# Optimization experiments

Measured on AMD Instinct MI355X. Metric: run time of the kernel, lower is better.

The kernel has to match this reference:

```python
import jax, jax.numpy as jnp
import numpy as np

B, T, H, W, D, NH = 8, 16, 14, 14, 768, 12
HID = int(D * 4.0)
HEAD_DIM = D // NH
EPS = 1e-5


def _ln(x, w, b):
    m = x.mean(-1, keepdims=True)
    v = ((x - m) ** 2).mean(-1, keepdims=True)
    return (x - m) * jax.lax.rsqrt(v + EPS) * w + b


def _attn(x, qkv_w, proj_w, proj_b):
    # x: [Bn, S, D]; qkv_w: [D, 3D] (no bias); proj: [D, D] + bias
    Bn, S, _ = x.shape
    qkv = (x @ qkv_w).reshape(Bn, S, 3, NH, HEAD_DIM).transpose(2, 0, 3, 1, 4)
    q, k, v = qkv[0], qkv[1], qkv[2]
    a = jnp.einsum('bhqd,bhkd->bhqk', q, k) * (HEAD_DIM ** -0.5)
    a = jax.nn.softmax(a, axis=-1)
    o = jnp.einsum('bhqk,bhkd->bhqd', a, v).transpose(0, 2, 1, 3).reshape(Bn, S, D)
    return o @ proj_w + proj_b


def setup_inputs() -> dict:
    key = jax.random.key(0)
    ks = jax.random.split(key, 20)
    N = H * W * T
    s = 0.02
    f32 = jnp.float32
    return {
        'x': jax.random.normal(ks[0], (B, 1 + N, D), f32),
        'tn1_w': jnp.ones((D,), f32), 'tn1_b': jnp.zeros((D,), f32),
        't_qkv_w': jax.random.normal(ks[1], (D, 3 * D), f32) * s,
        't_proj_w': jax.random.normal(ks[2], (D, D), f32) * s,
        't_proj_b': jnp.zeros((D,), f32),
        'tfc_w': jax.random.normal(ks[3], (D, D), f32) * s,
        'tfc_b': jnp.zeros((D,), f32),
        'n1_w': jnp.ones((D,), f32), 'n1_b': jnp.zeros((D,), f32),
        's_qkv_w': jax.random.normal(ks[4], (D, 3 * D), f32) * s,
        's_proj_w': jax.random.normal(ks[5], (D, D), f32) * s,
        's_proj_b': jnp.zeros((D,), f32),
        'n2_w': jnp.ones((D,), f32), 'n2_b': jnp.zeros((D,), f32),
        'fc1_w': jax.random.normal(ks[6], (D, HID), f32) * s,
        'fc1_b': jnp.zeros((HID,), f32),
        'fc2_w': jax.random.normal(ks[7], (HID, D), f32) * s,
        'fc2_b': jnp.zeros((D,), f32),
        'pt_mask': jnp.ones((B, 1 + N), dtype=bool),
        't_frames': T, 'height': H, 'width': W,
    }


def reference(x, tn1_w, tn1_b, t_qkv_w, t_proj_w, t_proj_b, tfc_w, tfc_b,
              n1_w, n1_b, s_qkv_w, s_proj_w, s_proj_b, n2_w, n2_b,
              fc1_w, fc1_b, fc2_w, fc2_b, pt_mask, t_frames, height, width):
    # divided space-time attention; USE_CLS_TOKEN=True, use_pt_visibility=False
    b = x.shape[0]
    t, h, w = t_frames, height, width
    n = h * w * t
    # --- temporal attention over t per (b, h, w) ---
    xt = x[:, 1:, :].reshape(b * h * w, t, D)  # 'b (h w t) m -> (b h w) t m'
    rt = _attn(_ln(xt, tn1_w, tn1_b), t_qkv_w, t_proj_w, t_proj_b)
    rt = rt.reshape(b, n, D) @ tfc_w + tfc_b  # temporal_fc
    xt2 = x[:, 1:, :] + rt
    init_cls = x[:, 0:1, :]  # [b, 1, D]
    # --- spatial attention over (1 + h*w) per (b, t) ---
    cls_tok = jnp.broadcast_to(init_cls, (b, t, D)).reshape(b * t, 1, D)
    xs = xt2.reshape(b, h * w, t, D).transpose(0, 2, 1, 3).reshape(b * t, h * w, D)
    xs = jnp.concatenate([cls_tok, xs], axis=1)  # [(b t), 1+hw, D]
    rs = _attn(_ln(xs, n1_w, n1_b), s_qkv_w, s_proj_w, s_proj_b)
    cls_out = rs[:, 0, :].reshape(b, t, D).mean(axis=1, keepdims=True)
    rs = rs[:, 1:, :].reshape(b, t, h * w, D).transpose(0, 2, 1, 3).reshape(b, n, D)
    x_new = jnp.concatenate([init_cls, xt2], axis=1) + jnp.concatenate([cls_out, rs], axis=1)
    # --- MLP block ---
    y = _ln(x_new, n2_w, n2_b)
    y = jax.nn.gelu(y @ fc1_w + fc1_b, approximate=False) @ fc2_w + fc2_b
    return x_new + y
```

## Files before the change

### kernel.cpp

```cpp
#include <hip/hip_runtime.h>
#include <cstdint>

using u16 = unsigned short;
using u32 = unsigned int;

typedef __bf16 bf16x8 __attribute__((ext_vector_type(8)));
typedef float  floatx4 __attribute__((ext_vector_type(4)));

#define DEV static __device__ __forceinline__

DEV u16 f2bf(float f) {
    u32 u = __float_as_uint(f);
    u += 0x7FFFu + ((u >> 16) & 1u);
    return (u16)(u >> 16);
}
DEV float bf2f(u16 v) { return __uint_as_float(((u32)v) << 16); }

DEV floatx4 mfma32(bf16x8 a, bf16x8 b, floatx4 c) {
    return __builtin_amdgcn_mfma_f32_16x16x32_bf16(a, b, c, 0, 0, 0);
}

DEV floatx4 fzero() { floatx4 z; z[0]=0.f; z[1]=0.f; z[2]=0.f; z[3]=0.f; return z; }

typedef __attribute__((address_space(3))) u32 as3_u32;
typedef __attribute__((address_space(1))) u32 as1_u32;

DEV void async_ld16(const u16* g, u16* l) {
    __builtin_amdgcn_global_load_lds(
        (const as1_u32*)g, (as3_u32*)l, 16, 0, 0);
}

__global__ __launch_bounds__(256) void transpose_w(
    const float* __restrict__ W, u16* __restrict__ Wt, int K, int N)
{
    __shared__ float t[32][33];
    const int tx = threadIdx.x, ty = threadIdx.y;
    const int gx = blockIdx.x * 32;
    const int gy = blockIdx.y * 32;
    #pragma unroll
    for (int i = 0; i < 4; ++i)
        t[ty + i*8][tx] = W[(size_t)(gy + ty + i*8) * N + gx + tx];
    __syncthreads();
    #pragma unroll
    for (int i = 0; i < 4; ++i)
        Wt[(size_t)(gx + ty + i*8) * K + gy + tx] = f2bf(t[tx][ty + i*8]);
}

__global__ __launch_bounds__(256) void cast_bf16(
    const float* __restrict__ W, u16* __restrict__ o, int n4)
{
    const int i = blockIdx.x * 256 + threadIdx.x;
    if (i < n4) {
        float4 v = reinterpret_cast<const float4*>(W)[i];
        union { u16 u[4]; uint2 q; } r;
        r.u[0]=f2bf(v.x); r.u[1]=f2bf(v.y); r.u[2]=f2bf(v.z); r.u[3]=f2bf(v.w);
        reinterpret_cast<uint2*>(o)[i] = r.q;
    }
}

__global__ __launch_bounds__(256) void fuse_bias(
    const float* __restrict__ pb, const float* __restrict__ Wf,
    const float* __restrict__ bf, float* __restrict__ bc)
{
    const int n = blockIdx.x * 4 + (threadIdx.x >> 6);
    const int lane = threadIdx.x & 63;
    float s = 0.f;
    #pragma unroll
    for (int it = 0; it < 12; ++it) {
        const int j = it*64 + lane;
        s += pb[j] * Wf[(size_t)j * 768 + n];
    }
    #pragma unroll
    for (int o = 32; o > 0; o >>= 1) s += __shfl_xor(s, o);
    if (lane == 0) bc[n] = s + bf[n];
}

template<int MODE>
__global__ __launch_bounds__(256) void ln_kernel(
    const float* __restrict__ xp, const u16* __restrict__ xt2,
    const float* __restrict__ w, const float* __restrict__ b,
    u16* __restrict__ out, int nrows)
{
    const int row = blockIdx.x * 4 + (threadIdx.x >> 6);
    if (row >= nrows) return;
    const int lane = threadIdx.x & 63;
    float vals[12];
    if constexpr (MODE == 0) {
        const float* src = xp + (size_t)(row + row/3136 + 1) * 768;
        #pragma unroll
        for (int j = 0; j < 3; ++j) {
            float4 v = reinterpret_cast<const float4*>(src)[j*64 + lane];
            vals[j*4+0]=v.x; vals[j*4+1]=v.y; vals[j*4+2]=v.z; vals[j*4+3]=v.w;
        }
    } else {
        const int bt = row / 197;
        const int p  = row - bt * 197;
        const int b0 = bt >> 4, tt = bt & 15;
        if (p == 0) {
            const float* src = xp + (size_t)b0 * 3137 * 768;
            #pragma unroll
            for (int j = 0; j < 3; ++j) {
                float4 v = reinterpret_cast<const float4*>(src)[j*64 + lane];
                vals[j*4+0]=v.x; vals[j*4+1]=v.y; vals[j*4+2]=v.z; vals[j*4+3]=v.w;
            }
        } else {
            const u16* src = xt2 + (size_t)(b0*3136 + (p-1)*16 + tt) * 768;
            #pragma unroll
            for (int j = 0; j < 3; ++j) {
                uint2 q = reinterpret_cast<const uint2*>(src)[j*64 + lane];
                vals[j*4+0] = bf2f((u16)(q.x & 0xFFFF));
                vals[j*4+1] = bf2f((u16)(q.x >> 16));
                vals[j*4+2] = bf2f((u16)(q.y & 0xFFFF));
                vals[j*4+3] = bf2f((u16)(q.y >> 16));
            }
        }
    }
    float s = 0.f, ss = 0.f;
    #pragma unroll
    for (int e = 0; e < 12; ++e) { s += vals[e]; ss += vals[e]*vals[e]; }
    #pragma unroll
    for (int o = 32; o > 0; o >>= 1) { s += __shfl_xor(s, o); ss += __shfl_xor(ss, o); }
    const float mean = s * (1.f/768.f);
    const float var  = ss * (1.f/768.f) - mean*mean;
    const float rstd = rsqrtf(var + 1e-5f);
    #pragma unroll
    for (int j = 0; j < 3; ++j) {
        const int c4 = (j*64 + lane) * 4;
        union { u16 u[4]; uint2 q; } o;
        #pragma unroll
        for (int e = 0; e < 4; ++e)
            o.u[e] = f2bf((vals[j*4+e] - mean)*rstd*w[c4+e] + b[c4+e]);
        *reinterpret_cast<uint2*>(&out[(size_t)row*768 + c4]) = o.q;
    }
}

__global__ __launch_bounds__(256) void combine_ln2(
    const float* __restrict__ xp, const u16* __restrict__ xt2,
    const u16* __restrict__ rsb, const float* __restrict__ w, const float* __restrict__ b,
    float* __restrict__ xnew, u16* __restrict__ ln2, int nrows)
{
    const int row = blockIdx.x * 4 + (threadIdx.x >> 6);
    if (row >= nrows) return;
    const int lane = threadIdx.x & 63;
    const int b0 = row / 3137;
    const int j  = row - b0 * 3137;
    float vals[12];
    if (j == 0) {
        #pragma unroll
        for (int e = 0; e < 12; ++e) {
            const int c = e*64 + lane;
            float acc = 0.f;
            for (int t = 0; t < 16; ++t)
                acc += bf2f(rsb[(size_t)(b0*16 + t) * 197 * 768 + c]);
            vals[e] = xp[(size_t)row*768 + c] + acc * (1.f/16.f);
        }
    } else {
        const int n_idx = j - 1;
        const int hw = n_idx >> 4, tt = n_idx & 15;
        const u16* a  = xt2 + (size_t)(b0*3136 + n_idx) * 768;
        const u16* r2 = rsb + (size_t)((b0*16 + tt)*197 + 1 + hw) * 768;
        #pragma unroll
        for (int e = 0; e < 12; ++e) {
            const int c = e*64 + lane;
            vals[e] = bf2f(a[c]) + bf2f(r2[c]);
        }
    }
    float s = 0.f, ss = 0.f;
    #pragma unroll
    for (int e = 0; e < 12; ++e) { s += vals[e]; ss += vals[e]*vals[e]; }
    #pragma unroll
    for (int o = 32; o > 0; o >>= 1) { s += __shfl_xor(s, o); ss += __shfl_xor(ss, o); }
    const float mean = s * (1.f/768.f);
    const float var  = ss * (1.f/768.f) - mean*mean;
    const float rstd = rsqrtf(var + 1e-5f);
    #pragma unroll
    for (int e = 0; e < 12; ++e) {
        const int c = e*64 + lane;
        xnew[(size_t)row*768 + c] = vals[e];
        ln2[(size_t)row*768 + c]  = f2bf((vals[e] - mean)*rstd*w[c] + b[c]);
    }
}

template<int RESID, bool BIAS, bool GELU_ACT, bool OUTF, bool OUTB, bool MASKM>
__global__ __launch_bounds__(256) void gemm_bt(
    const u16* __restrict__ A, const u16* __restrict__ Bt,
    const float* __restrict__ bias, const float* __restrict__ resid,
    float* __restrict__ Cf, u16* __restrict__ Cb,
    int N, int K, int lda, int ldb, int Mvalid)
{
    __shared__ __attribute__((aligned(16))) u16 smem[4*128*32];
    const int tid  = threadIdx.x;
    const int wave = tid >> 6;
    const int lane = tid & 63;
    const int m15  = lane & 15;
    const int quad = lane >> 4;
    const int wm = wave >> 1, wn = wave & 1;

    const int gx = (int)gridDim.x;
    const int nwg = gx * (int)gridDim.y;
    int lid = (int)blockIdx.y * gx + (int)blockIdx.x;
    {
        const int q = nwg >> 3, r = nwg & 7;
        const int c = lid & 7, idx = lid >> 3;
        lid = (c < r ? c*(q+1) : r*(q+1) + (c-r)*q) + idx;
    }
    const int bx = lid % gx;
    const int by = lid / gx;
    const long m0 = (long)by * 128;
    const long n0 = (long)bx * 128;

    const int s0 = wave*128 + lane;
    const int s1 = s0 + 64;
    const int kc0 = (s0 & 3) ^ ((s0 >> 3) & 3);
    const int kc1 = (s1 & 3) ^ ((s1 >> 3) & 3);
    const u16* Ag0 = A  + (size_t)(m0 + (s0 >> 2)) * lda + kc0 * 8;
    const u16* Ag1 = A  + (size_t)(m0 + (s1 >> 2)) * lda + kc1 * 8;
    const u16* Bg0 = Bt + (size_t)(n0 + (s0 >> 2)) * ldb + kc0 * 8;
    const u16* Bg1 = Bt + (size_t)(n0 + (s1 >> 2)) * ldb + kc1 * 8;

    const int swz = (quad ^ ((m15 >> 1) & 3)) * 8;

    floatx4 acc[4][4];
    #pragma unroll
    for (int i = 0; i < 4; ++i)
        #pragma unroll
        for (int j = 0; j < 4; ++j) acc[i][j] = fzero();

    auto stg = [&](int k0, int dn) {
        u16* base = smem + dn*8192;
        async_ld16(Ag0 + k0, base + (wave*2+0)*512);
        async_ld16(Ag1 + k0, base + (wave*2+1)*512);
        async_ld16(Bg0 + k0, base + 4096 + (wave*2+0)*512);
        async_ld16(Bg1 + k0, base + 4096 + (wave*2+1)*512);
    };
    auto comp = [&](int dn) {
        const u16* base = smem + dn*8192;
        bf16x8 af[4], bfr[4];
        #pragma unroll
        for (int i = 0; i < 4; ++i)
            af[i] = *reinterpret_cast<const bf16x8*>(&base[(wm*64 + i*16 + m15)*32 + swz]);
        #pragma unroll
        for (int j = 0; j < 4; ++j)
            bfr[j] = *reinterpret_cast<const bf16x8*>(&base[4096 + (wn*64 + j*16 + m15)*32 + swz]);
        #pragma unroll
        for (int i = 0; i < 4; ++i)
            #pragma unroll
            for (int j = 0; j < 4; ++j)
                acc[i][j] = mfma32(af[i], bfr[j], acc[i][j]);
    };

    const int NK = K >> 5;
    stg(0, 0);
    __syncthreads();
    for (int k = 0; k < NK; k += 2) {
        stg((k+1) << 5, 1);
        comp(0);
        __syncthreads();
        if (k + 2 < NK) stg((k+2) << 5, 0);
        comp(1);
        __syncthreads();
    }

    float bv[4];
    #pragma unroll
    for (int j = 0; j < 4; ++j)
        bv[j] = BIAS ? bias[n0 + wn*64 + j*16 + m15] : 0.f;

    if constexpr (OUTB) {
        u16* cbuf = smem + wave * 2048;
        #pragma unroll
        for (int p = 0; p < 2; ++p) {
            __syncthreads();
            #pragma unroll
            for (int ii = 0; ii < 2; ++ii) {
                const int i = p*2 + ii;
                #pragma unroll
                for (int j = 0; j < 4; ++j) {
                    #pragma unroll
                    for (int r = 0; r < 4; ++r) {
                        const long row = m0 + wm*64 + i*16 + quad*4 + r;
                        float v = acc[i][j][r] + bv[j];
                        if constexpr (RESID == 1)
                            v += resid[(size_t)row * N + (n0 + wn*64 + j*16 + m15)];
                        if constexpr (RESID == 2)
                            v += resid[(size_t)(row + row/3136 + 1) * 768 + (n0 + wn*64 + j*16 + m15)];
                        if constexpr (GELU_ACT)
                            v = 0.5f * v * (1.f + erff(v * 0.70710678118f));
                        cbuf[(ii*16 + quad*4 + r)*64 + j*16 + m15] = f2bf(v);
                    }
                }
            }
            __syncthreads();
            #pragma unroll
            for (int it = 0; it < 4; ++it) {
                const int lr = (lane >> 3) + it*8;
                const int cc = lane & 7;
                const uint4 val = *reinterpret_cast<const uint4*>(&cbuf[lr*64 + cc*8]);
                const long grow = m0 + wm*64 + p*32 + lr;
                *reinterpret_cast<uint4*>(&Cb[(size_t)grow * N + n0 + wn*64 + cc*8]) = val;
            }
        }
    } else {
        #pragma unroll
        for (int j = 0; j < 4; ++j) {
            const long col = n0 + wn*64 + j*16 + m15;
            #pragma unroll
            for (int i = 0; i < 4; ++i) {
                const long rowb = m0 + wm*64 + i*16 + quad*4;
                #pragma unroll
                for (int r = 0; r < 4; ++r) {
                    const long row = rowb + r;
                    if constexpr (MASKM) { if (row >= Mvalid) continue; }
                    float v = acc[i][j][r] + bv[j];
                    if constexpr (RESID == 1) v += resid[(size_t)row * N + col];
                    if constexpr (RESID == 2) v += resid[(size_t)(row + row/3136 + 1) * 768 + col];
                    if constexpr (GELU_ACT)   v = 0.5f * v * (1.f + erff(v * 0.70710678118f));
                    if constexpr (OUTF) Cf[(size_t)row * N + col] = v;
                }
            }
        }
    }
}

template<int S, int NQ, int NIT>
__global__ __launch_bounds__(256) void attn_kernel(
    const u16* __restrict__ qkv, u16* __restrict__ out, int ntask)
{
    __shared__ __attribute__((aligned(16))) u16 P_lds[4][16*32];
    const int wave = threadIdx.x >> 6;
    const int lane = threadIdx.x & 63;
    const int task = blockIdx.x * 4 + wave;
    if (task >= ntask) return;
    const int seq  = task / (12 * NQ);
    const int rem  = task - seq * (12 * NQ);
    const int head = rem / NQ;
    const int qt   = rem - head * NQ;
    const int m15  = lane & 15;
    const int quad = lane >> 4;
    const size_t base = (size_t)seq * S;

    const u16* qp = qkv + (base + qt*16 + m15) * 2304 + head*64 + quad*8;
    const bf16x8 Qf0 = *reinterpret_cast<const bf16x8*>(qp);
    const bf16x8 Qf1 = *reinterpret_cast<const bf16x8*>(qp + 32);

    floatx4 Oacc[4];
    #pragma unroll
    for (int c = 0; c < 4; ++c) Oacc[c] = fzero();
    float mrun = -__builtin_inff();
    float lrun = 0.f;
    u16* P = &P_lds[wave][0];

    for (int it = 0; it < NIT; ++it) {
        const int j0 = it * 32;
        floatx4 st[2];
        #pragma unroll
        for (int h2 = 0; h2 < 2; ++h2) {
            const u16* kp = qkv + (base + j0 + h2*16 + m15) * 2304 + 768 + head*64 + quad*8;
            const bf16x8 K0 = *reinterpret_cast<const bf16x8*>(kp);
            const bf16x8 K1 = *reinterpret_cast<const bf16x8*>(kp + 32);
            floatx4 z = fzero();
            z = mfma32(K0, Qf0, z);
            st[h2] = mfma32(K1, Qf1, z);
        }
        float sc[8];
        #pragma unroll
        for (int h2 = 0; h2 < 2; ++h2)
            #pragma unroll
            for (int r = 0; r < 4; ++r) {
                const int jj = j0 + h2*16 + quad*4 + r;
                sc[h2*4+r] = (jj < S) ? st[h2][r] * 0.125f : -__builtin_inff();
            }
        float tmax = sc[0];
        #pragma unroll
        for (int k = 1; k < 8; ++k) tmax = fmaxf(tmax, sc[k]);
        tmax = fmaxf(tmax, __shfl_xor(tmax, 16));
        tmax = fmaxf(tmax, __shfl_xor(tmax, 32));
        const float mnew = fmaxf(mrun, tmax);
        float p[8], tsum = 0.f;
        #pragma unroll
        for (int k = 0; k < 8; ++k) { p[k] = __expf(sc[k] - mnew); tsum += p[k]; }
        tsum += __shfl_xor(tsum, 16);
        tsum += __shfl_xor(tsum, 32);
        const float alpha = __expf(mrun - mnew);
        lrun = lrun * alpha + tsum;
        mrun = mnew;
        #pragma unroll
        for (int r = 0; r < 4; ++r) {
            const float ar = __shfl(alpha, quad*4 + r);
            #pragma unroll
            for (int c = 0; c < 4; ++c) Oacc[c][r] *= ar;
        }
        #pragma unroll
        for (int h2 = 0; h2 < 2; ++h2)
            #pragma unroll
            for (int r = 0; r < 4; ++r)
                P[m15*32 + h2*16 + quad*4 + r] = f2bf(p[h2*4+r]);
        const bf16x8 Pf = *reinterpret_cast<const bf16x8*>(&P[m15*32 + quad*8]);
        #pragma unroll
        for (int c = 0; c < 4; ++c) {
            union { u16 u[8]; bf16x8 v; } vf;
            #pragma unroll
            for (int jj2 = 0; jj2 < 8; ++jj2)
                vf.u[jj2] = qkv[(base + j0 + quad*8 + jj2) * 2304 + 1536 + head*64 + c*16 + m15];
            Oacc[c] = mfma32(Pf, vf.v, Oacc[c]);
        }
    }
    const float linv_self = 1.f / lrun;
    #pragma unroll
    for (int r = 0; r < 4; ++r) {
        const int prow = qt*16 + quad*4 + r;
        const float linv = __shfl(linv_self, quad*4 + r);
        if (prow < S) {
            u16* op = out + (base + prow) * 768 + head*64 + m15;
            #pragma unroll
            for (int c = 0; c < 4; ++c) op[c*16] = f2bf(Oacc[c][r] * linv);
        }
    }
}

extern "C" void kernel_launch(void* const* d_in, const int* in_sizes, int n_in,
                              void* d_out, int out_size, void* d_ws, size_t ws_size,
                              hipStream_t stream)
{
    (void)in_sizes; (void)n_in; (void)out_size; (void)ws_size;
    const float* x        = (const float*)d_in[0];
    const float* tn1_w    = (const float*)d_in[1];
    const float* tn1_b    = (const float*)d_in[2];
    const float* t_qkv_w  = (const float*)d_in[3];
    const float* t_proj_w = (const float*)d_in[4];
    const float* t_proj_b = (const float*)d_in[5];
    const float* tfc_w    = (const float*)d_in[6];
    const float* tfc_b    = (const float*)d_in[7];
    const float* n1_w     = (const float*)d_in[8];
    const float* n1_b     = (const float*)d_in[9];
    const float* s_qkv_w  = (const float*)d_in[10];
    const float* s_proj_w = (const float*)d_in[11];
    const float* s_proj_b = (const float*)d_in[12];
    const float* n2_w     = (const float*)d_in[13];
    const float* n2_b     = (const float*)d_in[14];
    const float* fc1_w    = (const float*)d_in[15];
    const float* fc1_b    = (const float*)d_in[16];
    const float* fc2_w    = (const float*)d_in[17];
    const float* fc2_b    = (const float*)d_in[18];
    float* out = (float*)d_out;

    char* ws = (char*)d_ws;
    size_t off = 0;
    auto alloc = [&](size_t bytes) -> void* {
        void* p = ws + off;
        off += (bytes + 255) & ~(size_t)255;
        return p;
    };
    u16* wt_tqkv  = (u16*)alloc((size_t)768*2304*2);
    u16* tproj_rm = (u16*)alloc((size_t)768*768*2);
    u16* wt_tfc   = (u16*)alloc((size_t)768*768*2);
    u16* wt_comb  = (u16*)alloc((size_t)768*768*2);
    float* bcomb  = (float*)alloc((size_t)768*4);
    u16* wt_sqkv  = (u16*)alloc((size_t)768*2304*2);
    u16* wt_sproj = (u16*)alloc((size_t)768*768*2);
    u16* wt_fc1   = (u16*)alloc((size_t)768*3072*2);
    u16* wt_fc2   = (u16*)alloc((size_t)3072*768*2);
    u16* slotA = (u16*)alloc((size_t)25280*2304*2);
    u16* slotB = (u16*)alloc((size_t)25216*768*2);
    u16* slotD = (u16*)alloc((size_t)25216*768*2);
    u16* slotE = (u16*)alloc((size_t)25216*768*2);

    dim3 tb(32, 8);
    transpose_w<<<dim3(72, 24), tb, 0, stream>>>(t_qkv_w,  wt_tqkv,  768, 2304);
    transpose_w<<<dim3(24, 24), tb, 0, stream>>>(tfc_w,    wt_tfc,   768, 768);
    transpose_w<<<dim3(72, 24), tb, 0, stream>>>(s_qkv_w,  wt_sqkv,  768, 2304);
    transpose_w<<<dim3(24, 24), tb, 0, stream>>>(s_proj_w, wt_sproj, 768, 768);
    transpose_w<<<dim3(96, 24), tb, 0, stream>>>(fc1_w,    wt_fc1,   768, 3072);
    transpose_w<<<dim3(24, 96), tb, 0, stream>>>(fc2_w,    wt_fc2,   3072, 768);
    cast_bf16<<<576, 256, 0, stream>>>(t_proj_w, tproj_rm, 768*768/4);

    gemm_bt<0,false,false,false,true,false><<<dim3(6,6), 256, 0, stream>>>(
        wt_tfc, tproj_rm, nullptr, nullptr, nullptr, wt_comb, 768, 768, 768, 768, 0);
    fuse_bias<<<192, 256, 0, stream>>>(t_proj_b, tfc_w, tfc_b, bcomb);

    u16* lnT  = slotD;
    u16* qkvT = slotA;
    ln_kernel<0><<<25088/4, 256, 0, stream>>>(x, nullptr, tn1_w, tn1_b, lnT, 25088);
    gemm_bt<0,false,false,false,true,false><<<dim3(18,196), 256, 0, stream>>>(
        lnT, wt_tqkv, nullptr, nullptr, nullptr, qkvT, 2304, 768, 768, 768, 0);

    u16* attnT = slotD;
    attn_kernel<16,1,1><<<18816/4, 256, 0, stream>>>(qkvT, attnT, 18816);

    u16* xt2 = slotB;
    gemm_bt<2,true,false,false,true,false><<<dim3(6,196), 256, 0, stream>>>(
        attnT, wt_comb, bcomb, x, nullptr, xt2, 768, 768, 768, 768, 0);

    u16* lnS = slotD;
    ln_kernel<1><<<25216/4, 256, 0, stream>>>(x, xt2, n1_w, n1_b, lnS, 25216);

    u16* qkvS = slotA;
    gemm_bt<0,false,false,false,true,false><<<dim3(18,197), 256, 0, stream>>>(
        lnS, wt_sqkv, nullptr, nullptr, nullptr, qkvS, 2304, 768, 768, 768, 0);

    u16* attnS = slotD;
    attn_kernel<197,13,7><<<19968/4, 256, 0, stream>>>(qkvS, attnS, 19968);

    u16* rsb = slotE;
    gemm_bt<0,true,false,false,true,false><<<dim3(6,197), 256, 0, stream>>>(
        attnS, wt_sproj, s_proj_b, nullptr, nullptr, rsb, 768, 768, 768, 768, 0);

    float* xnew = out;
    u16* ln2 = slotD;
    combine_ln2<<<25096/4, 256, 0, stream>>>(x, xt2, rsb, n2_w, n2_b, xnew, ln2, 25096);

    u16* h1 = slotA;
    for (int half = 0; half < 2; ++half) {
        const u16* w1h = wt_fc1 + (size_t)half * 1536 * 768;
        const float* b1h = fc1_b + half * 1536;
        gemm_bt<0,true,true,false,true,false><<<dim3(12,197), 256, 0, stream>>>(
            ln2, w1h, b1h, nullptr, nullptr, h1, 1536, 768, 768, 768, 0);
        const u16* w2h = wt_fc2 + (size_t)half * 1536;
        if (half == 0)
            gemm_bt<1,true,false,true,false,true><<<dim3(6,197), 256, 0, stream>>>(
                h1, w2h, fc2_b, out, out, nullptr, 768, 1536, 1536, 3072, 25096);
        else
            gemm_bt<1,false,false,true,false,true><<<dim3(6,197), 256, 0, stream>>>(
                h1, w2h, nullptr, out, out, nullptr, 768, 1536, 1536, 3072, 25096);
    }
}
```

Before: 1.302 ms.

## Load GEMM fragments directly from global memory into registers, bypassing LDS

The GEMM kernel drops the async global-to-LDS staging and the shared-memory double buffer. Each wave now loads its MFMA operand fragments straight from global memory into registers, with a two-stage register prefetch. This removes the block-wide barriers and LDS reads in the main loop, and the epilogue barriers. In exchange, each operand row is fetched by multiple waves, raising L1/L2 traffic, and the loads are narrow strided row accesses.

```diff
diff --git a/kernel.cpp b/kernel.cpp
--- a/kernel.cpp
+++ b/kernel.cpp
@@ -21,14 +21,6 @@
 }
 
 DEV floatx4 fzero() { floatx4 z; z[0]=0.f; z[1]=0.f; z[2]=0.f; z[3]=0.f; return z; }
-
-typedef __attribute__((address_space(3))) u32 as3_u32;
-typedef __attribute__((address_space(1))) u32 as1_u32;
-
-DEV void async_ld16(const u16* g, u16* l) {
-    __builtin_amdgcn_global_load_lds(
-        (const as1_u32*)g, (as3_u32*)l, 16, 0, 0);
-}
 
 __global__ __launch_bounds__(256) void transpose_w(
     const float* __restrict__ W, u16* __restrict__ Wt, int K, int N)
@@ -182,13 +174,13 @@
 }
 
 template<int RESID, bool BIAS, bool GELU_ACT, bool OUTF, bool OUTB, bool MASKM>
-__global__ __launch_bounds__(256) void gemm_bt(
+__global__ __launch_bounds__(256) void gemm_l2(
     const u16* __restrict__ A, const u16* __restrict__ Bt,
     const float* __restrict__ bias, const float* __restrict__ resid,
     float* __restrict__ Cf, u16* __restrict__ Cb,
     int N, int K, int lda, int ldb, int Mvalid)
 {
-    __shared__ __attribute__((aligned(16))) u16 smem[4*128*32];
+    __shared__ __attribute__((aligned(16))) u16 cbuf_all[4*2048];
     const int tid  = threadIdx.x;
     const int wave = tid >> 6;
     const int lane = tid & 63;
@@ -209,16 +201,12 @@
     const long m0 = (long)by * 128;
     const long n0 = (long)bx * 128;
 
-    const int s0 = wave*128 + lane;
-    const int s1 = s0 + 64;
-    const int kc0 = (s0 & 3) ^ ((s0 >> 3) & 3);
-    const int kc1 = (s1 & 3) ^ ((s1 >> 3) & 3);
-    const u16* Ag0 = A  + (size_t)(m0 + (s0 >> 2)) * lda + kc0 * 8;
-    const u16* Ag1 = A  + (size_t)(m0 + (s1 >> 2)) * lda + kc1 * 8;
-    const u16* Bg0 = Bt + (size_t)(n0 + (s0 >> 2)) * ldb + kc0 * 8;
-    const u16* Bg1 = Bt + (size_t)(n0 + (s1 >> 2)) * ldb + kc1 * 8;
-
-    const int swz = (quad ^ ((m15 >> 1) & 3)) * 8;
+    const u16* pAf[4]; const u16* pBf[4];
+    #pragma unroll
+    for (int f = 0; f < 4; ++f) {
+        pAf[f] = A  + (size_t)(m0 + wm*64 + f*16 + m15) * lda + quad*8;
+        pBf[f] = Bt + (size_t)(n0 + wn*64 + f*16 + m15) * ldb + quad*8;
+    }
 
     floatx4 acc[4][4];
     #pragma unroll
@@ -226,51 +214,45 @@
         #pragma unroll
         for (int j = 0; j < 4; ++j) acc[i][j] = fzero();
 
-    auto stg = [&](int k0, int dn) {
-        u16* base = smem + dn*8192;
-        async_ld16(Ag0 + k0, base + (wave*2+0)*512);
-        async_ld16(Ag1 + k0, base + (wave*2+1)*512);
-        async_ld16(Bg0 + k0, base + 4096 + (wave*2+0)*512);
-        async_ld16(Bg1 + k0, base + 4096 + (wave*2+1)*512);
+    bf16x8 a0[4], b0[4], a1[4], b1[4];
+    auto LD = [&](bf16x8* av, bf16x8* bv, int k0) {
+        #pragma unroll
+        for (int f = 0; f < 4; ++f)
+            av[f] = *reinterpret_cast<const bf16x8*>(pAf[f] + k0);
+        #pragma unroll
+        for (int f = 0; f < 4; ++f)
+            bv[f] = *reinterpret_cast<const bf16x8*>(pBf[f] + k0);
     };
-    auto comp = [&](int dn) {
-        const u16* base = smem + dn*8192;
-        bf16x8 af[4], bfr[4];
+    auto MM = [&](bf16x8* av, bf16x8* bv) {
         #pragma unroll
         for (int i = 0; i < 4; ++i)
-            af[i] = *reinterpret_cast<const bf16x8*>(&base[(wm*64 + i*16 + m15)*32 + swz]);
-        #pragma unroll
-        for (int j = 0; j < 4; ++j)
-            bfr[j] = *reinterpret_cast<const bf16x8*>(&base[4096 + (wn*64 + j*16 + m15)*32 + swz]);
-        #pragma unroll
-        for (int i = 0; i < 4; ++i)
             #pragma unroll
             for (int j = 0; j < 4; ++j)
-                acc[i][j] = mfma32(af[i], bfr[j], acc[i][j]);
+                acc[i][j] = mfma32(av[i], bv[j], acc[i][j]);
     };
 
-    const int NK = K >> 5;
-    stg(0, 0);
-    __syncthreads();
-    for (int k = 0; k < NK; k += 2) {
-        stg((k+1) << 5, 1);
-        comp(0);
-        __syncthreads();
-        if (k + 2 < NK) stg((k+2) << 5, 0);
-        comp(1);
-        __syncthreads();
-    }
-
-    float bv[4];
+    const int NK2 = K >> 6;
+    LD(a0, b0, 0);
+    int k0 = 0;
+    for (int it = 0; it < NK2 - 1; ++it, k0 += 64) {
+        LD(a1, b1, k0 + 32);
+        MM(a0, b0);
+        LD(a0, b0, k0 + 64);
+        MM(a1, b1);
+    }
+    LD(a1, b1, k0 + 32);
+    MM(a0, b0);
+    MM(a1, b1);
+
+    float bv4[4];
     #pragma unroll
     for (int j = 0; j < 4; ++j)
-        bv[j] = BIAS ? bias[n0 + wn*64 + j*16 + m15] : 0.f;
+        bv4[j] = BIAS ? bias[n0 + wn*64 + j*16 + m15] : 0.f;
 
     if constexpr (OUTB) {
-        u16* cbuf = smem + wave * 2048;
+        u16* cbuf = cbuf_all + wave * 2048;
         #pragma unroll
         for (int p = 0; p < 2; ++p) {
-            __syncthreads();
             #pragma unroll
             for (int ii = 0; ii < 2; ++ii) {
                 const int i = p*2 + ii;
@@ -279,7 +261,7 @@
                     #pragma unroll
                     for (int r = 0; r < 4; ++r) {
                         const long row = m0 + wm*64 + i*16 + quad*4 + r;
-                        float v = acc[i][j][r] + bv[j];
+                        float v = acc[i][j][r] + bv4[j];
                         if constexpr (RESID == 1)
                             v += resid[(size_t)row * N + (n0 + wn*64 + j*16 + m15)];
                         if constexpr (RESID == 2)
@@ -290,7 +272,6 @@
                     }
                 }
             }
-            __syncthreads();
             #pragma unroll
             for (int it = 0; it < 4; ++it) {
                 const int lr = (lane >> 3) + it*8;
@@ -311,7 +292,7 @@
                 for (int r = 0; r < 4; ++r) {
                     const long row = rowb + r;
                     if constexpr (MASKM) { if (row >= Mvalid) continue; }
-                    float v = acc[i][j][r] + bv[j];
+                    float v = acc[i][j][r] + bv4[j];
                     if constexpr (RESID == 1) v += resid[(size_t)row * N + col];
                     if constexpr (RESID == 2) v += resid[(size_t)(row + row/3136 + 1) * 768 + col];
                     if constexpr (GELU_ACT)   v = 0.5f * v * (1.f + erff(v * 0.70710678118f));
@@ -474,35 +455,35 @@
     transpose_w<<<dim3(24, 96), tb, 0, stream>>>(fc2_w,    wt_fc2,   3072, 768);
     cast_bf16<<<576, 256, 0, stream>>>(t_proj_w, tproj_rm, 768*768/4);
 
-    gemm_bt<0,false,false,false,true,false><<<dim3(6,6), 256, 0, stream>>>(
+    gemm_l2<0,false,false,false,true,false><<<dim3(6,6), 256, 0, stream>>>(
         wt_tfc, tproj_rm, nullptr, nullptr, nullptr, wt_comb, 768, 768, 768, 768, 0);
     fuse_bias<<<192, 256, 0, stream>>>(t_proj_b, tfc_w, tfc_b, bcomb);
 
     u16* lnT  = slotD;
     u16* qkvT = slotA;
     ln_kernel<0><<<25088/4, 256, 0, stream>>>(x, nullptr, tn1_w, tn1_b, lnT, 25088);
-    gemm_bt<0,false,false,false,true,false><<<dim3(18,196), 256, 0, stream>>>(
+    gemm_l2<0,false,false,false,true,false><<<dim3(18,196), 256, 0, stream>>>(
         lnT, wt_tqkv, nullptr, nullptr, nullptr, qkvT, 2304, 768, 768, 768, 0);
 
     u16* attnT = slotD;
     attn_kernel<16,1,1><<<18816/4, 256, 0, stream>>>(qkvT, attnT, 18816);
 
     u16* xt2 = slotB;
-    gemm_bt<2,true,false,false,true,false><<<dim3(6,196), 256, 0, stream>>>(
+    gemm_l2<2,true,false,false,true,false><<<dim3(6,196), 256, 0, stream>>>(
         attnT, wt_comb, bcomb, x, nullptr, xt2, 768, 768, 768, 768, 0);
 
     u16* lnS = slotD;
     ln_kernel<1><<<25216/4, 256, 0, stream>>>(x, xt2, n1_w, n1_b, lnS, 25216);
 
     u16* qkvS = slotA;
-    gemm_bt<0,false,false,false,true,false><<<dim3(18,197), 256, 0, stream>>>(
+    gemm_l2<0,false,false,false,true,false><<<dim3(18,197), 256, 0, stream>>>(
         lnS, wt_sqkv, nullptr, nullptr, nullptr, qkvS, 2304, 768, 768, 768, 0);
 
     u16* attnS = slotD;
     attn_kernel<197,13,7><<<19968/4, 256, 0, stream>>>(qkvS, attnS, 19968);
 
     u16* rsb = slotE;
-    gemm_bt<0,true,false,false,true,false><<<dim3(6,197), 256, 0, stream>>>(
+    gemm_l2<0,true,false,false,true,false><<<dim3(6,197), 256, 0, stream>>>(
         attnS, wt_sproj, s_proj_b, nullptr, nullptr, rsb, 768, 768, 768, 768, 0);
 
     float* xnew = out;
@@ -513,14 +494,14 @@
     for (int half = 0; half < 2; ++half) {
         const u16* w1h = wt_fc1 + (size_t)half * 1536 * 768;
         const float* b1h = fc1_b + half * 1536;
-        gemm_bt<0,true,true,false,true,false><<<dim3(12,197), 256, 0, stream>>>(
+        gemm_l2<0,true,true,false,true,false><<<dim3(12,197), 256, 0, stream>>>(
             ln2, w1h, b1h, nullptr, nullptr, h1, 1536, 768, 768, 768, 0);
         const u16* w2h = wt_fc2 + (size_t)half * 1536;
         if (half == 0)
-            gemm_bt<1,true,false,true,false,true><<<dim3(6,197), 256, 0, stream>>>(
+            gemm_l2<1,true,false,true,false,true><<<dim3(6,197), 256, 0, stream>>>(
                 h1, w2h, fc2_b, out, out, nullptr, 768, 1536, 1536, 3072, 25096);
         else
-            gemm_bt<1,false,false,true,false,true><<<dim3(6,197), 256, 0, stream>>>(
+            gemm_l2<1,false,false,true,false,true><<<dim3(6,197), 256, 0, stream>>>(
                 h1, w2h, nullptr, out, out, nullptr, 768, 1536, 1536, 3072, 25096);
     }
 }
```

Result: slower. 2.379 ms (+82.8%).

## Replace 4-wave 128x128 GEMM with single-wave 64x64 barrier-free GEMM

Applied to the files above, without the earlier changes.

Each GEMM workgroup becomes one 64-thread wave computing a 64x64 tile. Double-buffered LDS staging is synchronised with explicit vmcnt waits instead of __syncthreads, with a two-stage prefetch, and grids are resized to match. This removes workgroup barriers and shrinks LDS per block so more blocks fit per CU. In exchange, each block reuses less data per load, which raises global/L2 traffic, and the vmcnt-only waits rely on each lane reading only LDS it staged itself.

```diff
diff --git a/kernel.cpp b/kernel.cpp
--- a/kernel.cpp
+++ b/kernel.cpp
@@ -181,22 +181,24 @@
     }
 }
 
+#define WAITV8() do { asm volatile("s_waitcnt vmcnt(8)" ::: "memory"); \
+    __builtin_amdgcn_sched_barrier(0); } while(0)
+#define WAITVZ() do { asm volatile("s_waitcnt vmcnt(0)" ::: "memory"); \
+    __builtin_amdgcn_sched_barrier(0); } while(0)
+
 template<int RESID, bool BIAS, bool GELU_ACT, bool OUTF, bool OUTB, bool MASKM>
-__global__ __launch_bounds__(256) void gemm_bt(
+__global__ __launch_bounds__(64) void gemm_w(
     const u16* __restrict__ A, const u16* __restrict__ Bt,
     const float* __restrict__ bias, const float* __restrict__ resid,
     float* __restrict__ Cf, u16* __restrict__ Cb,
     int N, int K, int lda, int ldb, int Mvalid)
 {
-    __shared__ __attribute__((aligned(16))) u16 smem[4*128*32];
-    const int tid  = threadIdx.x;
-    const int wave = tid >> 6;
-    const int lane = tid & 63;
+    __shared__ __attribute__((aligned(16))) u16 smem[8192];
+    const int lane = threadIdx.x;
     const int m15  = lane & 15;
     const int quad = lane >> 4;
-    const int wm = wave >> 1, wn = wave & 1;
-
-    const int gx = (int)gridDim.x;
+
+    const int gx  = (int)gridDim.x;
     const int nwg = gx * (int)gridDim.y;
     int lid = (int)blockIdx.y * gx + (int)blockIdx.x;
     {
@@ -206,17 +208,24 @@
     }
     const int bx = lid % gx;
     const int by = lid / gx;
-    const long m0 = (long)by * 128;
-    const long n0 = (long)bx * 128;
-
-    const int s0 = wave*128 + lane;
-    const int s1 = s0 + 64;
-    const int kc0 = (s0 & 3) ^ ((s0 >> 3) & 3);
-    const int kc1 = (s1 & 3) ^ ((s1 >> 3) & 3);
-    const u16* Ag0 = A  + (size_t)(m0 + (s0 >> 2)) * lda + kc0 * 8;
-    const u16* Ag1 = A  + (size_t)(m0 + (s1 >> 2)) * lda + kc1 * 8;
-    const u16* Bg0 = Bt + (size_t)(n0 + (s0 >> 2)) * ldb + kc0 * 8;
-    const u16* Bg1 = Bt + (size_t)(n0 + (s1 >> 2)) * ldb + kc1 * 8;
+    const long m0 = (long)by * 64;
+    const long n0 = (long)bx * 64;
+
+    const u16* gA[4]; const u16* gB[4];
+    #pragma unroll
+    for (int i = 0; i < 4; ++i) {
+        const int s  = i*64 + lane;
+        const int kc = (s & 3) ^ ((s >> 3) & 3);
+        gA[i] = A  + (size_t)(m0 + (s >> 2)) * lda + kc*8;
+        gB[i] = Bt + (size_t)(n0 + (s >> 2)) * ldb + kc*8;
+    }
+    auto stg = [&](int k0, int d) {
+        u16* base = smem + d*4096;
+        #pragma unroll
+        for (int i = 0; i < 4; ++i) async_ld16(gA[i] + k0, base + i*512);
+        #pragma unroll
+        for (int i = 0; i < 4; ++i) async_ld16(gB[i] + k0, base + 2048 + i*512);
+    };
 
     const int swz = (quad ^ ((m15 >> 1) & 3)) * 8;
 
@@ -226,22 +235,15 @@
         #pragma unroll
         for (int j = 0; j < 4; ++j) acc[i][j] = fzero();
 
-    auto stg = [&](int k0, int dn) {
-        u16* base = smem + dn*8192;
-        async_ld16(Ag0 + k0, base + (wave*2+0)*512);
-        async_ld16(Ag1 + k0, base + (wave*2+1)*512);
-        async_ld16(Bg0 + k0, base + 4096 + (wave*2+0)*512);
-        async_ld16(Bg1 + k0, base + 4096 + (wave*2+1)*512);
-    };
-    auto comp = [&](int dn) {
-        const u16* base = smem + dn*8192;
+    auto comp = [&](int d) {
+        const u16* base = smem + d*4096;
         bf16x8 af[4], bfr[4];
         #pragma unroll
-        for (int i = 0; i < 4; ++i)
-            af[i] = *reinterpret_cast<const bf16x8*>(&base[(wm*64 + i*16 + m15)*32 + swz]);
+        for (int f = 0; f < 4; ++f)
+            af[f] = *reinterpret_cast<const bf16x8*>(&base[(f*16 + m15)*32 + swz]);
         #pragma unroll
         for (int j = 0; j < 4; ++j)
-            bfr[j] = *reinterpret_cast<const bf16x8*>(&base[4096 + (wn*64 + j*16 + m15)*32 + swz]);
+            bfr[j] = *reinterpret_cast<const bf16x8*>(&base[2048 + (j*16 + m15)*32 + swz]);
         #pragma unroll
         for (int i = 0; i < 4; ++i)
             #pragma unroll
@@ -251,26 +253,30 @@
 
     const int NK = K >> 5;
     stg(0, 0);
-    __syncthreads();
-    for (int k = 0; k < NK; k += 2) {
-        stg((k+1) << 5, 1);
+    stg(32, 1);
+    #pragma unroll 1
+    for (int t = 0; t + 4 <= NK; t += 2) {
+        WAITV8();
         comp(0);
-        __syncthreads();
-        if (k + 2 < NK) stg((k+2) << 5, 0);
+        __builtin_amdgcn_sched_barrier(0);
+        stg((t + 2) << 5, 0);
+        WAITV8();
         comp(1);
-        __syncthreads();
-    }
+        __builtin_amdgcn_sched_barrier(0);
+        stg((t + 3) << 5, 1);
+    }
+    WAITV8();  comp(0);
+    WAITVZ();  comp(1);
 
     float bv[4];
     #pragma unroll
     for (int j = 0; j < 4; ++j)
-        bv[j] = BIAS ? bias[n0 + wn*64 + j*16 + m15] : 0.f;
+        bv[j] = BIAS ? bias[n0 + j*16 + m15] : 0.f;
 
     if constexpr (OUTB) {
-        u16* cbuf = smem + wave * 2048;
+        u16* cbuf = smem;
         #pragma unroll
         for (int p = 0; p < 2; ++p) {
-            __syncthreads();
             #pragma unroll
             for (int ii = 0; ii < 2; ++ii) {
                 const int i = p*2 + ii;
@@ -278,35 +284,37 @@
                 for (int j = 0; j < 4; ++j) {
                     #pragma unroll
                     for (int r = 0; r < 4; ++r) {
-                        const long row = m0 + wm*64 + i*16 + quad*4 + r;
+                        const long row = m0 + i*16 + quad*4 + r;
                         float v = acc[i][j][r] + bv[j];
                         if constexpr (RESID == 1)
-                            v += resid[(size_t)row * N + (n0 + wn*64 + j*16 + m15)];
+                            v += resid[(size_t)row * N + (n0 + j*16 + m15)];
                         if constexpr (RESID == 2)
-                            v += resid[(size_t)(row + row/3136 + 1) * 768 + (n0 + wn*64 + j*16 + m15)];
+                            v += resid[(size_t)(row + row/3136 + 1) * 768 + (n0 + j*16 + m15)];
                         if constexpr (GELU_ACT)
                             v = 0.5f * v * (1.f + erff(v * 0.70710678118f));
                         cbuf[(ii*16 + quad*4 + r)*64 + j*16 + m15] = f2bf(v);
                     }
                 }
             }
-            __syncthreads();
             #pragma unroll
             for (int it = 0; it < 4; ++it) {
                 const int lr = (lane >> 3) + it*8;
                 const int cc = lane & 7;
                 const uint4 val = *reinterpret_cast<const uint4*>(&cbuf[lr*64 + cc*8]);
-                const long grow = m0 + wm*64 + p*32 + lr;
-                *reinterpret_cast<uint4*>(&Cb[(size_t)grow * N + n0 + wn*64 + cc*8]) = val;
+                const long grow = m0 + p*32 + lr;
+                bool ok = true;
+                if constexpr (MASKM) ok = (grow < Mvalid);
+                if (ok)
+                    *reinterpret_cast<uint4*>(&Cb[(size_t)grow * N + n0 + cc*8]) = val;
             }
         }
     } else {
         #pragma unroll
         for (int j = 0; j < 4; ++j) {
-            const long col = n0 + wn*64 + j*16 + m15;
+            const long col = n0 + j*16 + m15;
             #pragma unroll
             for (int i = 0; i < 4; ++i) {
-                const long rowb = m0 + wm*64 + i*16 + quad*4;
+                const long rowb = m0 + i*16 + quad*4;
                 #pragma unroll
                 for (int r = 0; r < 4; ++r) {
                     const long row = rowb + r;
@@ -474,35 +482,35 @@
     transpose_w<<<dim3(24, 96), tb, 0, stream>>>(fc2_w,    wt_fc2,   3072, 768);
     cast_bf16<<<576, 256, 0, stream>>>(t_proj_w, tproj_rm, 768*768/4);
 
-    gemm_bt<0,false,false,false,true,false><<<dim3(6,6), 256, 0, stream>>>(
+    gemm_w<0,false,false,false,true,false><<<dim3(12,12), 64, 0, stream>>>(
         wt_tfc, tproj_rm, nullptr, nullptr, nullptr, wt_comb, 768, 768, 768, 768, 0);
     fuse_bias<<<192, 256, 0, stream>>>(t_proj_b, tfc_w, tfc_b, bcomb);
 
     u16* lnT  = slotD;
     u16* qkvT = slotA;
     ln_kernel<0><<<25088/4, 256, 0, stream>>>(x, nullptr, tn1_w, tn1_b, lnT, 25088);
-    gemm_bt<0,false,false,false,true,false><<<dim3(18,196), 256, 0, stream>>>(
+    gemm_w<0,false,false,false,true,false><<<dim3(36,392), 64, 0, stream>>>(
         lnT, wt_tqkv, nullptr, nullptr, nullptr, qkvT, 2304, 768, 768, 768, 0);
 
     u16* attnT = slotD;
     attn_kernel<16,1,1><<<18816/4, 256, 0, stream>>>(qkvT, attnT, 18816);
 
     u16* xt2 = slotB;
-    gemm_bt<2,true,false,false,true,false><<<dim3(6,196), 256, 0, stream>>>(
+    gemm_w<2,true,false,false,true,false><<<dim3(12,392), 64, 0, stream>>>(
         attnT, wt_comb, bcomb, x, nullptr, xt2, 768, 768, 768, 768, 0);
 
     u16* lnS = slotD;
     ln_kernel<1><<<25216/4, 256, 0, stream>>>(x, xt2, n1_w, n1_b, lnS, 25216);
 
     u16* qkvS = slotA;
-    gemm_bt<0,false,false,false,true,false><<<dim3(18,197), 256, 0, stream>>>(
+    gemm_w<0,false,false,false,true,false><<<dim3(36,394), 64, 0, stream>>>(
         lnS, wt_sqkv, nullptr, nullptr, nullptr, qkvS, 2304, 768, 768, 768, 0);
 
     u16* attnS = slotD;
     attn_kernel<197,13,7><<<19968/4, 256, 0, stream>>>(qkvS, attnS, 19968);
 
     u16* rsb = slotE;
-    gemm_bt<0,true,false,false,true,false><<<dim3(6,197), 256, 0, stream>>>(
+    gemm_w<0,true,false,false,true,false><<<dim3(12,394), 64, 0, stream>>>(
         attnS, wt_sproj, s_proj_b, nullptr, nullptr, rsb, 768, 768, 768, 768, 0);
 
     float* xnew = out;
@@ -513,14 +521,14 @@
     for (int half = 0; half < 2; ++half) {
         const u16* w1h = wt_fc1 + (size_t)half * 1536 * 768;
         const float* b1h = fc1_b + half * 1536;
-        gemm_bt<0,true,true,false,true,false><<<dim3(12,197), 256, 0, stream>>>(
+        gemm_w<0,true,true,false,true,false><<<dim3(24,393), 64, 0, stream>>>(
             ln2, w1h, b1h, nullptr, nullptr, h1, 1536, 768, 768, 768, 0);
         const u16* w2h = wt_fc2 + (size_t)half * 1536;
         if (half == 0)
-            gemm_bt<1,true,false,true,false,true><<<dim3(6,197), 256, 0, stream>>>(
+            gemm_w<1,true,false,true,false,true><<<dim3(12,393), 64, 0, stream>>>(
                 h1, w2h, fc2_b, out, out, nullptr, 768, 1536, 1536, 3072, 25096);
         else
-            gemm_bt<1,false,false,true,false,true><<<dim3(6,197), 256, 0, stream>>>(
+            gemm_w<1,false,false,true,false,true><<<dim3(12,393), 64, 0, stream>>>(
                 h1, w2h, nullptr, out, out, nullptr, 768, 1536, 1536, 3072, 25096);
     }
 }
```

Measured after the change: 1.575 ms. 1.21x slower.
